# Kernel tuning notes

Measured on AMD Instinct MI355X. Metric: run time of the kernel, lower is better.

The kernel has to match this reference:

```python
import jax, jax.numpy as jnp
import numpy as np

B, L, D_MODEL, D_K, HEADS, C = 4, 4096, 512, 64, 8, 2
TOPK = int(C * np.log(L))  # int(c * log(input_seq_len)) = 16


def setup_inputs() -> dict:
    key = jax.random.key(0)
    ks = jax.random.split(key, 5)
    q_in = jax.random.normal(ks[0], (B, L, D_MODEL), jnp.float32)
    k_in = jax.random.normal(ks[1], (B, L, D_MODEL), jnp.float32)
    v_in = jax.random.normal(ks[2], (B, L, D_MODEL), jnp.float32)
    Wq = jax.random.normal(ks[3], (D_MODEL, D_K), jnp.float32) / np.sqrt(D_MODEL)
    bq = jax.random.normal(ks[4], (D_K,), jnp.float32) * 0.01
    return {"q_in": q_in, "k_in": k_in, "v_in": v_in, "Wq": Wq, "bq": bq}


def _to_heads(x, Wq, bq):
    # Faithful to original: ALL of q/k/v use the `query` Dense layer, and all
    # heads are identical copies (same projection stacked `heads` times).
    p = x @ Wq + bq                       # [B, L, d_k]
    p = jnp.swapaxes(p, 1, 2)             # [B, d_k, L]  (transpose [0,3,2,1] of [B,L,d,H])
    return jnp.broadcast_to(p[:, None], (p.shape[0], HEADS, D_K, p.shape[-1]))  # [B,H,d,L]


def reference(q_in, k_in, v_in, Wq, bq):
    Q = jnp.fft.fft(_to_heads(q_in, Wq, bq).astype(jnp.complex64), axis=-1)
    K = jnp.fft.fft(_to_heads(k_in, Wq, bq).astype(jnp.complex64), axis=-1)
    V = _to_heads(v_in, Wq, bq)           # [B,H,d,L] float32
    QK = jnp.fft.ifft(Q * jnp.conj(K), axis=-1)   # circular cross-correlation
    qk_abs = jnp.abs(QK)                  # [B,H,d,L]

    vals, idx = jax.lax.top_k(qk_abs, TOPK)       # [B,H,d,k]
    w = jax.nn.softmax(vals, axis=-1)             # softmax over the k lags

    # tf.roll(v, shift=-lag): out[t] = v[(t + lag) mod L]  -> vectorized gather
    t = jnp.arange(L, dtype=jnp.int32)
    gidx = (idx[..., None] + t) % L               # [B,H,d,k,L]
    Vk = jnp.broadcast_to(V[:, :, :, None, :], gidx.shape)
    rolled = jnp.take_along_axis(Vk, gidx, axis=-1)           # [B,H,d,k,L]
    agg = jnp.sum(rolled * w[..., None], axis=3)              # [B,H,d,L]

    out = agg.reshape(agg.shape[0], HEADS * D_K, L)           # [B, H*d, L]
    return jnp.transpose(out, (0, 2, 1))                      # [B, L, H*d]
```

## Files before the change

### kernel.cpp

```cpp
#include <hip/hip_runtime.h>
#include <hip/hip_bf16.h>

#define BQ 4
#define LQ 4096
#define DM 512
#define DK 64
#define NROWS (BQ * DK)
#define TOPK 16
#define CAND 32

typedef __attribute__((ext_vector_type(8))) short short8v;
typedef __attribute__((ext_vector_type(16))) float f32x16;

__device__ __forceinline__ unsigned short f2bf(float x) {
  unsigned u = __builtin_bit_cast(unsigned, x);
  return (unsigned short)((u + 0x7FFFu + ((u >> 16) & 1u)) >> 16);
}
__device__ __forceinline__ float bf2f(unsigned short h) {
  unsigned u = ((unsigned)h) << 16;
  return __builtin_bit_cast(float, u);
}

__device__ __forceinline__ void mfma_drain() {
  __builtin_amdgcn_sched_barrier(0);
  asm volatile("s_nop 7\n\ts_nop 7\n\ts_nop 7\n\ts_nop 7" ::: "memory");
  __builtin_amdgcn_sched_barrier(0);
}

__global__ __launch_bounds__(256) void wprep_kernel(
    const float* __restrict__ Wq, short* __restrict__ wpack) {
  const int ks = blockIdx.x;
  const int t = threadIdx.x;
  const int lane = t & 63, half = t >> 6;
  const int plane = half >> 1, nt = half & 1;
  const int r = nt * 32 + (lane & 31);
  const int kb = 16 * ks + 8 * (lane >> 5);
  short8v o;
#pragma unroll
  for (int i = 0; i < 8; ++i) {
    float v = Wq[(size_t)(kb + i) * DK + r];
    unsigned short h = f2bf(v);
    o[i] = plane ? (short)f2bf(v - bf2f(h)) : (short)h;
  }
  *(short8v*)(&wpack[(((size_t)plane * 2 + nt) * 32 + ks) * 512 + lane * 8]) = o;
}

__global__ __launch_bounds__(256, 3) void proj_kernel(
    const float* __restrict__ q_in, const float* __restrict__ k_in,
    const float* __restrict__ v_in, const short* __restrict__ wpack,
    const float* __restrict__ bq, float* __restrict__ ws) {
  const float* x = blockIdx.z == 0 ? q_in : (blockIdx.z == 1 ? k_in : v_in);
  float* outp = ws + (size_t)blockIdx.z * (size_t)(NROWS * LQ);

  __shared__ __align__(16) float smem[4352];

  const int tid = threadIdx.x;
  const int l = tid & 63, wv = tid >> 6;
  const int tile = wv >> 1, kh = wv & 1;
  const int R0 = blockIdx.x * 64 + tile * 32;
  const int koff = 8 * (l >> 5);

  const float* xb = x + (size_t)(R0 + (l & 31)) * DM + kh * 256 + koff;
  const short* wp0 = wpack + l * 8;

  f32x16 acc[2];
#pragma unroll
  for (int nt = 0; nt < 2; ++nt)
#pragma unroll
    for (int i = 0; i < 16; ++i) acc[nt][i] = 0.f;

  float4 a0[8], a1[8];
#pragma unroll
  for (int s = 0; s < 4; ++s) {
    a0[2 * s]     = *(const float4*)(xb + s * 16);
    a0[2 * s + 1] = *(const float4*)(xb + s * 16 + 4);
  }

  short8v wc[4], wn[4];
#define WLOAD(dst, ksl)                                                      \
  do {                                                                       \
    const int kg = kh * 16 + (ksl);                                          \
    dst[0] = *(const short8v*)(wp0 + ((kg + 0) << 9));                       \
    dst[1] = *(const short8v*)(wp0 + ((kg + 64) << 9));                      \
    dst[2] = *(const short8v*)(wp0 + ((kg + 32) << 9));                      \
    dst[3] = *(const short8v*)(wp0 + ((kg + 96) << 9));                      \
  } while (0)
  WLOAD(wc, 0);

#pragma unroll
  for (int kb = 0; kb < 4; ++kb) {
    if (kb < 3) {
#pragma unroll
      for (int s = 0; s < 4; ++s) {
        a1[2 * s]     = *(const float4*)(xb + (kb + 1) * 64 + s * 16);
        a1[2 * s + 1] = *(const float4*)(xb + (kb + 1) * 64 + s * 16 + 4);
      }
    }
#pragma unroll
    for (int s = 0; s < 4; ++s) {
      const int ksl = kb * 4 + s;
      if (ksl < 15) WLOAD(wn, ksl + 1);
      float f[8] = {a0[2 * s].x, a0[2 * s].y, a0[2 * s].z, a0[2 * s].w,
                    a0[2 * s + 1].x, a0[2 * s + 1].y, a0[2 * s + 1].z,
                    a0[2 * s + 1].w};
      short8v ah, al;
#pragma unroll
      for (int i = 0; i < 8; ++i) {
        unsigned short h = f2bf(f[i]);
        ah[i] = (short)h;
        al[i] = (short)f2bf(f[i] - bf2f(h));
      }
      asm volatile(
          "s_nop 4\n\t"
          "v_mfma_f32_32x32x16_bf16 %0, %2, %4, %0\n\t"
          "v_mfma_f32_32x32x16_bf16 %0, %2, %5, %0\n\t"
          "v_mfma_f32_32x32x16_bf16 %0, %3, %4, %0\n\t"
          "v_mfma_f32_32x32x16_bf16 %1, %2, %6, %1\n\t"
          "v_mfma_f32_32x32x16_bf16 %1, %2, %7, %1\n\t"
          "v_mfma_f32_32x32x16_bf16 %1, %3, %6, %1\n\t"
          "s_nop 7\n\t"
          "s_nop 3"
          : "+v"(acc[0]), "+v"(acc[1])
          : "v"(ah), "v"(al), "v"(wc[0]), "v"(wc[1]), "v"(wc[2]), "v"(wc[3]));
      if (ksl < 15) {
#pragma unroll
        for (int i = 0; i < 4; ++i) wc[i] = wn[i];
      }
    }
    if (kb < 3) {
#pragma unroll
      for (int i = 0; i < 8; ++i) a0[i] = a1[i];
    }
  }
#undef WLOAD

  mfma_drain();
  if (kh == 1) {
#pragma unroll
    for (int nt = 0; nt < 2; ++nt)
#pragma unroll
      for (int r = 0; r < 16; ++r)
        smem[tile * 2048 + nt * 1024 + r * 64 + l] = acc[nt][r];
  }
  __syncthreads();
  if (kh == 0) {
#pragma unroll
    for (int nt = 0; nt < 2; ++nt)
#pragma unroll
      for (int r = 0; r < 16; ++r)
        acc[nt][r] += smem[tile * 2048 + nt * 1024 + r * 64 + l];
  }
  __syncthreads();

  if (kh == 0) {
    const int b = R0 >> 12, i0 = R0 & (LQ - 1);
    float bb[2] = {bq[l & 31], bq[32 + (l & 31)]};
#pragma unroll
    for (int nt = 0; nt < 2; ++nt) {
      float* area = smem + (tile * 2 + nt) * 1088;
#pragma unroll
      for (int r = 0; r < 16; ++r) {
        int io = (r & 3) + 8 * (r >> 2) + 4 * (l >> 5);
        area[(l & 31) * 34 + io] = acc[nt][r] + bb[nt];
      }
      const int e = l & 15, jg = l >> 4;
#pragma unroll
      for (int p = 0; p < 8; ++p) {
        int jj = jg * 8 + p;
        float2 v = *reinterpret_cast<const float2*>(area + jj * 34 + e * 2);
        *reinterpret_cast<float2*>(
            &outp[((size_t)b * DK + nt * 32 + jj) * LQ + i0 + e * 2]) = v;
      }
    }
  }
}

__global__ __launch_bounds__(512) void corr_topk_kernel(
    const float* __restrict__ qp, const float* __restrict__ kp,
    float* __restrict__ lw) {
  const int row = blockIdx.x;
  const int tid = threadIdx.x;
  __shared__ __align__(16) short qs[3 * 4112 + 4096];
  __shared__ __align__(16) short ks[4096];
  __shared__ __align__(16) float qf[LQ];
  __shared__ __align__(16) float kf[LQ];
  __shared__ unsigned wk[128];
  __shared__ unsigned scand[CAND];
  __shared__ float rS[CAND];
  __shared__ float ordv[TOPK]; __shared__ int ordl[TOPK];

  const float* qr = qp + ((size_t)row << 12);
  const float* kr = kp + ((size_t)row << 12);

  {
    const float4* q4 = (const float4*)qr;
    float4 v0 = q4[tid * 2], v1 = q4[tid * 2 + 1];
    float4 v2 = q4[(tid * 2 + 2) & 1023];
    ((float4*)qf)[tid * 2] = v0;
    ((float4*)qf)[tid * 2 + 1] = v1;
    float f[12] = {v0.x, v0.y, v0.z, v0.w, v1.x, v1.y, v1.z, v1.w,
                   v2.x, v2.y, v2.z, v2.w};
#pragma unroll
    for (int r = 0; r < 4; ++r) {
      short8v o;
#pragma unroll
      for (int i = 0; i < 8; ++i) o[i] = (short)f2bf(f[i + r]);
      *(short8v*)(&qs[r * 4112 + tid * 8]) = o;
    }
    const float4* k4 = (const float4*)kr;
    float4 w0 = k4[tid * 2], w1 = k4[tid * 2 + 1];
    ((float4*)kf)[tid * 2] = w0;
    ((float4*)kf)[tid * 2 + 1] = w1;
    float g[8] = {w0.x, w0.y, w0.z, w0.w, w1.x, w1.y, w1.z, w1.w};
    int Q = tid;
    int Qs = Q ^ ((Q >> 3) & 7);
    short8v o;
#pragma unroll
    for (int i = 0; i < 8; ++i) o[i] = (short)f2bf(g[i]);
    *(short8v*)(&ks[Qs << 3]) = o;
  }
  __syncthreads();

  const int l = tid & 63, wv = tid >> 6;
  const int Oq = ((8 * (l >> 5) - 32 * (l & 31)) & 4095) >> 3;
  const int rB = (l & 31) & 3;
  const int Ce = (l & 31) + 8 * (l >> 5) - rB;
  const short* qb = qs + rB * 4112;

  f32x16 acc[4];
#pragma unroll
  for (int M = 0; M < 4; ++M)
#pragma unroll
    for (int i = 0; i < 16; ++i) acc[M][i] = 0.f;

  const int J0 = wv * 32;
#pragma unroll 2
  for (int jb = 0; jb < 32; ++jb) {
    const int J = J0 + jb;
    int e1 = (Ce + 16 * J) & 4095;
    int e2 = (e1 + 4) & 4095;
    uint2 blo = *(const uint2*)(qb + e1);
    uint2 bhi = *(const uint2*)(qb + e2);
    int4 bi; bi.x = blo.x; bi.y = blo.y; bi.z = bhi.x; bi.w = bhi.y;
    short8v bf = __builtin_bit_cast(short8v, bi);
    const int Dq = 2 * J;
#pragma unroll
    for (int M = 0; M < 4; ++M) {
      int Q = (Oq + Dq - 128 * M) & 511;
      Q ^= (Q >> 3) & 7;
      short8v af = *(const short8v*)(&ks[Q << 3]);
      asm volatile("v_mfma_f32_32x32x16_bf16 %0, %1, %2, %0"
                   : "+v"(acc[M]) : "v"(af), "v"(bf));
    }
  }

  mfma_drain();
  __syncthreads();
  float* red = (float*)qs;
  const int strip = (wv & 1) * 4096;
  const int ch4 = (l >> 5) * 4, cn = l & 31;
#define RIDX(M, r) (strip + ((M) << 10) + 32 * (((r)&3) + 8 * ((r) >> 2) + ch4) + cn)
  if (wv < 2) {
#pragma unroll
    for (int M = 0; M < 4; ++M)
#pragma unroll
      for (int r = 0; r < 16; ++r) red[RIDX(M, r)] = acc[M][r];
  }
  __syncthreads();
  if (wv >= 2 && wv < 4) {
#pragma unroll
    for (int M = 0; M < 4; ++M)
#pragma unroll
      for (int r = 0; r < 16; ++r) red[RIDX(M, r)] += acc[M][r];
  }
  __syncthreads();
  if (wv >= 4 && wv < 6) {
#pragma unroll
    for (int M = 0; M < 4; ++M)
#pragma unroll
      for (int r = 0; r < 16; ++r) red[RIDX(M, r)] += acc[M][r];
  }
  __syncthreads();
  if (wv >= 6) {
#pragma unroll
    for (int M = 0; M < 4; ++M)
#pragma unroll
      for (int r = 0; r < 16; ++r) red[RIDX(M, r)] += acc[M][r];
  }
  __syncthreads();
#undef RIDX

  {
    unsigned key[8];
#pragma unroll
    for (int i = 0; i < 8; ++i) {
      int tau = wv * 512 + i * 64 + l;
      float v = red[tau] + red[4096 + tau];
      unsigned u = __builtin_bit_cast(unsigned, fabsf(v));
      key[i] = (u & 0xFFFFF000u) | (unsigned)(4095 - tau);
    }
    unsigned bkey = key[0];
#pragma unroll
    for (int i = 1; i < 8; ++i) bkey = key[i] > bkey ? key[i] : bkey;
    for (int round = 0; round < 16; ++round) {
      unsigned m = bkey;
#pragma unroll
      for (int off = 1; off < 64; off <<= 1) {
        unsigned o = __shfl_xor(m, off);
        m = o > m ? o : m;
      }
      if (l == 0) wk[wv * 16 + round] = m;
#pragma unroll
      for (int i = 0; i < 8; ++i) key[i] = (key[i] == m) ? 0u : key[i];
      bkey = key[0];
#pragma unroll
      for (int i = 1; i < 8; ++i) bkey = key[i] > bkey ? key[i] : bkey;
    }
  }
  __syncthreads();

  if (tid < 128) {
    unsigned ki = wk[tid];
    int rank = 0;
    for (int j = 0; j < 128; ++j) rank += (wk[j] > ki);
    if (rank < CAND) scand[rank] = ki;
  }
  __syncthreads();

  {
    const int ci = tid >> 4, sub = tid & 15;
    const int lag = 4095 - (int)(scand[ci] & 0xFFFu);
    float S0 = 0.f, S1 = 0.f, S2 = 0.f, S3 = 0.f;
    for (int it = 0; it < 256; it += 4) {
      int t0 = (it + 0) * 16 + sub, t1 = (it + 1) * 16 + sub;
      int t2 = (it + 2) * 16 + sub, t3 = (it + 3) * 16 + sub;
      S0 = fmaf(kf[t0], qf[(t0 + lag) & 4095], S0);
      S1 = fmaf(kf[t1], qf[(t1 + lag) & 4095], S1);
      S2 = fmaf(kf[t2], qf[(t2 + lag) & 4095], S2);
      S3 = fmaf(kf[t3], qf[(t3 + lag) & 4095], S3);
    }
    float S = (S0 + S1) + (S2 + S3);
    S += __shfl_xor(S, 1);
    S += __shfl_xor(S, 2);
    S += __shfl_xor(S, 4);
    S += __shfl_xor(S, 8);
    if (sub == 0) rS[ci] = S;
  }
  __syncthreads();

  if (tid < CAND) {
    float vi = fabsf(rS[tid]);
    int ii = 4095 - (int)(scand[tid] & 0xFFFu);
    int rank = 0;
    for (int j = 0; j < CAND; ++j) {
      float vj = fabsf(rS[j]);
      int ij = 4095 - (int)(scand[j] & 0xFFFu);
      rank += (vj > vi) || (vj == vi && ij < ii);
    }
    if (rank < TOPK) { ordv[rank] = vi; ordl[rank] = ii; }
  }
  __syncthreads();

  if (tid == 0) {
    float m0 = ordv[0], s = 0.f, e[TOPK];
    for (int k = 0; k < TOPK; ++k) { e[k] = expf(ordv[k] - m0); s += e[k]; }
    float inv = 1.f / s;
    int* ip = (int*)(lw + (size_t)row * 32);
    for (int k = 0; k < TOPK; ++k) {
      ip[k] = ordl[k];
      ((float*)ip)[TOPK + k] = e[k] * inv;
    }
  }
}

__global__ void agg_kernel(const float* __restrict__ vpT,
                           const float* __restrict__ lw,
                           float* __restrict__ aggT) {
  const int row = blockIdx.x, tid = threadIdx.x;
  __shared__ __align__(16) float vr[2 * LQ];
  __shared__ float w[TOPK]; __shared__ int lg[TOPK];

  const float* v0 = vpT + (size_t)row * LQ;
  for (int x = tid; x < LQ; x += 256) {
    float val = v0[x];
    vr[x] = val; vr[x + LQ] = val;
  }
  if (tid < TOPK) {
    lg[tid] = ((const int*)(lw + (size_t)row * 32))[tid];
    w[tid] = lw[(size_t)row * 32 + TOPK + tid];
  }
  __syncthreads();

  float wr[TOPK]; int lr[TOPK];
#pragma unroll
  for (int k = 0; k < TOPK; ++k) { wr[k] = w[k]; lr[k] = lg[k]; }

  for (int m = 0; m < 16; ++m) {
    int t = m * 256 + tid;
    float a = 0.f;
#pragma unroll
    for (int k = 0; k < TOPK; ++k) a = fmaf(wr[k], vr[t + lr[k]], a);
    aggT[(size_t)row * LQ + t] = a;
  }
}

__global__ void trans_kernel(const float* __restrict__ aggT,
                             float* __restrict__ out) {
  const int b = blockIdx.y;
  const int t0 = blockIdx.x * 64;
  const int tid = threadIdx.x;
  __shared__ float ts[64][65];

#pragma unroll
  for (int v = 0; v < 16; ++v) {
    int f = v * 256 + tid;
    int d = f >> 6, tt = f & 63;
    ts[d][tt] = aggT[((size_t)b * DK + d) * LQ + t0 + tt];
  }
  __syncthreads();

#pragma unroll
  for (int v = 0; v < 128; ++v) {
    int f = v * 256 + tid;
    int tt = f >> 9, c = f & 511;
    out[((size_t)b * LQ + t0 + tt) * (8 * DK) + c] = ts[c & 63][tt];
  }
}

extern "C" void kernel_launch(void* const* d_in, const int* in_sizes, int n_in,
                              void* d_out, int out_size, void* d_ws, size_t ws_size,
                              hipStream_t stream) {
  const float* q_in = (const float*)d_in[0];
  const float* k_in = (const float*)d_in[1];
  const float* v_in = (const float*)d_in[2];
  const float* Wq   = (const float*)d_in[3];
  const float* bq   = (const float*)d_in[4];
  float* out = (float*)d_out;
  float* ws  = (float*)d_ws;

  const size_t M = (size_t)NROWS * LQ;
  float* qp    = ws;
  float* kp    = ws + M;
  float* vp    = ws + 2 * M;
  float* lw    = ws + 3 * M;
  float* aggT  = ws + 4 * M;
  short* wpack = (short*)(ws + 5 * M);

  wprep_kernel<<<32, 256, 0, stream>>>(Wq, wpack);
  proj_kernel<<<dim3(256, 1, 3), 256, 0, stream>>>(q_in, k_in, v_in, wpack,
                                                   bq, ws);
  corr_topk_kernel<<<NROWS, 512, 0, stream>>>(qp, kp, lw);
  agg_kernel<<<NROWS, 256, 0, stream>>>(vp, lw, aggT);
  trans_kernel<<<dim3(LQ / 64, BQ), 256, 0, stream>>>(aggT, out);
}
```

Baseline: 75.31 us.

## Software-pipeline projection loads with inline-asm global loads and explicit vmcnt waits

Rewrites the projection GEMM main loop to issue global loads through inline assembly. X tiles are double-buffered and weight fragments triple-buffered, prefetched two k-slices ahead, with hand-counted s_waitcnt vmcnt values so each MFMA group waits only for its own data. Occupancy hint drops from 3 to 2 blocks per SU to make room for the extra buffer registers. This aims to hide global memory latency better, but it risks stalls if the vmcnt accounting is off and loses latency hiding from fewer resident waves.

Result: no change. 75.46 us (+0.2%).

```diff
diff --git a/kernel.cpp b/kernel.cpp
--- a/kernel.cpp
+++ b/kernel.cpp
@@ -9,6 +9,7 @@
 #define TOPK 16
 #define CAND 32
 
+typedef __attribute__((ext_vector_type(4))) float f32x4;
 typedef __attribute__((ext_vector_type(8))) short short8v;
 typedef __attribute__((ext_vector_type(16))) float f32x16;
 
@@ -26,6 +27,13 @@
   asm volatile("s_nop 7\n\ts_nop 7\n\ts_nop 7\n\ts_nop 7" ::: "memory");
   __builtin_amdgcn_sched_barrier(0);
 }
+
+#define VMCNT_(n) asm volatile("s_waitcnt vmcnt(" #n ")" ::: "memory")
+#define VMCNT(n)                        \
+  do {                                  \
+    VMCNT_(n);                          \
+    __builtin_amdgcn_sched_barrier(0);  \
+  } while (0)
 
 __global__ __launch_bounds__(256) void wprep_kernel(
     const float* __restrict__ Wq, short* __restrict__ wpack) {
@@ -45,7 +53,60 @@
   *(short8v*)(&wpack[(((size_t)plane * 2 + nt) * 32 + ks) * 512 + lane * 8]) = o;
 }
 
-__global__ __launch_bounds__(256, 3) void proj_kernel(
+#define XLOAD(buf, kb_)                                                        \
+  do {                                                                         \
+    const float* xbase_ = xb + (kb_) * 64;                                     \
+    asm volatile("global_load_dwordx4 %0, %1, off" : "=v"(buf[0]) : "v"(xbase_));            \
+    asm volatile("global_load_dwordx4 %0, %1, off offset:16" : "=v"(buf[1]) : "v"(xbase_));  \
+    asm volatile("global_load_dwordx4 %0, %1, off offset:64" : "=v"(buf[2]) : "v"(xbase_));  \
+    asm volatile("global_load_dwordx4 %0, %1, off offset:80" : "=v"(buf[3]) : "v"(xbase_));  \
+    asm volatile("global_load_dwordx4 %0, %1, off offset:128" : "=v"(buf[4]) : "v"(xbase_)); \
+    asm volatile("global_load_dwordx4 %0, %1, off offset:144" : "=v"(buf[5]) : "v"(xbase_)); \
+    asm volatile("global_load_dwordx4 %0, %1, off offset:192" : "=v"(buf[6]) : "v"(xbase_)); \
+    asm volatile("global_load_dwordx4 %0, %1, off offset:208" : "=v"(buf[7]) : "v"(xbase_)); \
+  } while (0)
+
+#define WLOADR(buf, ksl_)                                                      \
+  do {                                                                         \
+    const short* wb_ = wp0 + ((size_t)(kh * 16 + (ksl_)) << 9);                \
+    asm volatile("global_load_dwordx4 %0, %1, off" : "=v"(buf[0]) : "v"(wb_)); \
+    asm volatile("global_load_dwordx4 %0, %1, off" : "=v"(buf[1]) : "v"(wb_ + (64 << 9))); \
+    asm volatile("global_load_dwordx4 %0, %1, off" : "=v"(buf[2]) : "v"(wb_ + (32 << 9))); \
+    asm volatile("global_load_dwordx4 %0, %1, off" : "=v"(buf[3]) : "v"(wb_ + (96 << 9))); \
+  } while (0)
+
+#define STEP(kb_, s_, vm_)                                                     \
+  do {                                                                         \
+    if ((s_) == 0 && (kb_) < 3) XLOAD(xr[((kb_) + 1) & 1], (kb_) + 1);         \
+    if (4 * (kb_) + (s_) < 14) WLOADR(wr3[(4 * (kb_) + (s_) + 2) % 3],         \
+                                      4 * (kb_) + (s_) + 2);                   \
+    VMCNT(vm_);                                                                \
+    const f32x4* xa_ = xr[(kb_) & 1] + 2 * (s_);                               \
+    float f_[8] = {xa_[0][0], xa_[0][1], xa_[0][2], xa_[0][3],                 \
+                   xa_[1][0], xa_[1][1], xa_[1][2], xa_[1][3]};                \
+    short8v ah_, al_;                                                          \
+    _Pragma("unroll")                                                          \
+    for (int i_ = 0; i_ < 8; ++i_) {                                           \
+      unsigned short h_ = f2bf(f_[i_]);                                        \
+      ah_[i_] = (short)h_;                                                     \
+      al_[i_] = (short)f2bf(f_[i_] - bf2f(h_));                                \
+    }                                                                          \
+    short8v* w_ = wr3[(4 * (kb_) + (s_)) % 3];                                 \
+    asm volatile(                                                              \
+        "s_nop 4\n\t"                                                          \
+        "v_mfma_f32_32x32x16_bf16 %0, %2, %4, %0\n\t"                          \
+        "v_mfma_f32_32x32x16_bf16 %0, %2, %5, %0\n\t"                          \
+        "v_mfma_f32_32x32x16_bf16 %0, %3, %4, %0\n\t"                          \
+        "v_mfma_f32_32x32x16_bf16 %1, %2, %6, %1\n\t"                          \
+        "v_mfma_f32_32x32x16_bf16 %1, %2, %7, %1\n\t"                          \
+        "v_mfma_f32_32x32x16_bf16 %1, %3, %6, %1\n\t"                          \
+        "s_nop 7\n\t"                                                          \
+        "s_nop 3"                                                              \
+        : "+v"(acc[0]), "+v"(acc[1])                                           \
+        : "v"(ah_), "v"(al_), "v"(w_[0]), "v"(w_[1]), "v"(w_[2]), "v"(w_[3])); \
+  } while (0)
+
+__global__ __launch_bounds__(256, 2) void proj_kernel(
     const float* __restrict__ q_in, const float* __restrict__ k_in,
     const float* __restrict__ v_in, const short* __restrict__ wpack,
     const float* __restrict__ bq, float* __restrict__ ws) {
@@ -69,70 +130,17 @@
 #pragma unroll
     for (int i = 0; i < 16; ++i) acc[nt][i] = 0.f;
 
-  float4 a0[8], a1[8];
-#pragma unroll
-  for (int s = 0; s < 4; ++s) {
-    a0[2 * s]     = *(const float4*)(xb + s * 16);
-    a0[2 * s + 1] = *(const float4*)(xb + s * 16 + 4);
-  }
-
-  short8v wc[4], wn[4];
-#define WLOAD(dst, ksl)                                                      \
-  do {                                                                       \
-    const int kg = kh * 16 + (ksl);                                          \
-    dst[0] = *(const short8v*)(wp0 + ((kg + 0) << 9));                       \
-    dst[1] = *(const short8v*)(wp0 + ((kg + 64) << 9));                      \
-    dst[2] = *(const short8v*)(wp0 + ((kg + 32) << 9));                      \
-    dst[3] = *(const short8v*)(wp0 + ((kg + 96) << 9));                      \
-  } while (0)
-  WLOAD(wc, 0);
-
-#pragma unroll
-  for (int kb = 0; kb < 4; ++kb) {
-    if (kb < 3) {
-#pragma unroll
-      for (int s = 0; s < 4; ++s) {
-        a1[2 * s]     = *(const float4*)(xb + (kb + 1) * 64 + s * 16);
-        a1[2 * s + 1] = *(const float4*)(xb + (kb + 1) * 64 + s * 16 + 4);
-      }
-    }
-#pragma unroll
-    for (int s = 0; s < 4; ++s) {
-      const int ksl = kb * 4 + s;
-      if (ksl < 15) WLOAD(wn, ksl + 1);
-      float f[8] = {a0[2 * s].x, a0[2 * s].y, a0[2 * s].z, a0[2 * s].w,
-                    a0[2 * s + 1].x, a0[2 * s + 1].y, a0[2 * s + 1].z,
-                    a0[2 * s + 1].w};
-      short8v ah, al;
-#pragma unroll
-      for (int i = 0; i < 8; ++i) {
-        unsigned short h = f2bf(f[i]);
-        ah[i] = (short)h;
-        al[i] = (short)f2bf(f[i] - bf2f(h));
-      }
-      asm volatile(
-          "s_nop 4\n\t"
-          "v_mfma_f32_32x32x16_bf16 %0, %2, %4, %0\n\t"
-          "v_mfma_f32_32x32x16_bf16 %0, %2, %5, %0\n\t"
-          "v_mfma_f32_32x32x16_bf16 %0, %3, %4, %0\n\t"
-          "v_mfma_f32_32x32x16_bf16 %1, %2, %6, %1\n\t"
-          "v_mfma_f32_32x32x16_bf16 %1, %2, %7, %1\n\t"
-          "v_mfma_f32_32x32x16_bf16 %1, %3, %6, %1\n\t"
-          "s_nop 7\n\t"
-          "s_nop 3"
-          : "+v"(acc[0]), "+v"(acc[1])
-          : "v"(ah), "v"(al), "v"(wc[0]), "v"(wc[1]), "v"(wc[2]), "v"(wc[3]));
-      if (ksl < 15) {
-#pragma unroll
-        for (int i = 0; i < 4; ++i) wc[i] = wn[i];
-      }
-    }
-    if (kb < 3) {
-#pragma unroll
-      for (int i = 0; i < 8; ++i) a0[i] = a1[i];
-    }
-  }
-#undef WLOAD
+  f32x4 xr[2][8];
+  short8v wr3[3][4];
+
+  XLOAD(xr[0], 0);
+  WLOADR(wr3[0], 0);
+  WLOADR(wr3[1], 1);
+
+  STEP(0, 0, 16); STEP(0, 1, 16); STEP(0, 2, 8);  STEP(0, 3, 8);
+  STEP(1, 0, 16); STEP(1, 1, 16); STEP(1, 2, 8);  STEP(1, 3, 8);
+  STEP(2, 0, 16); STEP(2, 1, 16); STEP(2, 2, 8);  STEP(2, 3, 8);
+  STEP(3, 0, 8);  STEP(3, 1, 8);  STEP(3, 2, 4);  STEP(3, 3, 0);
 
   mfma_drain();
   if (kh == 1) {
```
